# Kernel optimization log

Hardware: AMD Instinct MI355X
Metric: run time of the kernel (lower is better)

The kernel has to match this reference:

```python
import jax, jax.numpy as jnp
import numpy as np

N_NODES = 50000
DEG = 32
HEADS = 4
OUT_F = 16
IN_F = 64
NEG_SLOPE = 0.01  # jax.nn.leaky_relu default


def setup_inputs() -> dict:
    key = jax.random.key(0)
    k_adj, k_mask, k_q, k_qw, k_kw, k_aw = jax.random.split(key, 6)
    adj = jax.random.randint(k_adj, (N_NODES, DEG), 0, N_NODES)
    pad = jax.random.uniform(k_mask, (N_NODES, DEG)) < 0.1
    adj = jnp.where(pad, -1, adj)
    Q = jax.random.normal(k_q, (IN_F, N_NODES), dtype=jnp.float32)
    qw_scale = 2 * np.sqrt(6.0 / (IN_F + OUT_F * HEADS))
    kw_scale = qw_scale
    a_scale = 2 * np.sqrt(6.0 / (OUT_F + HEADS))
    query_weight = (jax.random.uniform(k_qw, (HEADS, OUT_F, IN_F)) - 0.5) * qw_scale
    key_weight = (jax.random.uniform(k_kw, (HEADS, OUT_F, IN_F)) - 0.5) * kw_scale
    attn_weight = (jax.random.uniform(k_aw, (HEADS, OUT_F)) - 0.5) * a_scale
    return {
        'adj': adj,
        'Q': Q,
        'query_weight': query_weight.astype(jnp.float32),
        'key_weight': key_weight.astype(jnp.float32),
        'attn_weight': attn_weight.astype(jnp.float32),
    }


def reference(adj, Q, query_weight, key_weight, attn_weight):
    # K defaults to Q (self-attention over graph)
    K = Q
    # project keys: [H, O, N], then gather neighbors -> [H, O, N, deg]
    Ko = jnp.einsum('hoi,in->hon', key_weight, K)[..., adj]
    # project queries: [H, O, N]
    Qo = jnp.einsum('hoi,in->hon', query_weight, Q)
    # per-edge pre-activation and attention logits
    X = jax.nn.leaky_relu(Qo[..., None] + Ko, negative_slope=NEG_SLOPE)
    X = jnp.einsum('honk,ho->hnk', X, attn_weight)  # [H, N, deg]
    X = jnp.where(adj == -1, -jnp.inf, X)
    # rows with zero valid neighbors -> zero logits (uniform softmax, masked later)
    X = jnp.where((adj != -1).sum(-1, keepdims=True) == 0, 0.0, X)
    attn = jax.nn.softmax(X, axis=-1)
    # weighted aggregate of gathered keys -> [H, O, N]
    return jnp.einsum('hnk,honk->hon', jnp.where(adj == -1, 0.0, attn), Ko)
```

## Files before the change

kernel.cpp:

```cpp
#include <hip/hip_runtime.h>
#include <math.h>

#define DEG 32
#define NHO 64
#define NPW 4
#define NPB 16

typedef short  frag8  __attribute__((ext_vector_type(8)));
typedef float  f32x4  __attribute__((ext_vector_type(4)));

template <int CTRL>
__device__ __forceinline__ float dpp_add(float v) {
    int t = __builtin_amdgcn_update_dpp(0, __float_as_int(v), CTRL, 0xF, 0xF, true);
    return v + __int_as_float(t);
}

__device__ __forceinline__ unsigned bf16_rne(float f) {
    unsigned u = __float_as_uint(f);
    return (u + 0x7fffu + ((u >> 16) & 1u)) >> 16;
}

__global__ __launch_bounds__(256) void proj_mfma_kernel(
    const float* __restrict__ Q,
    const float* __restrict__ Wq,
    const float* __restrict__ Wk,
    float* __restrict__ Pq,
    unsigned short* __restrict__ Pkb,
    int N)
{
    __shared__ unsigned qlds[64 * 33];
    __shared__ unsigned wlds[128 * 33];

    int t  = threadIdx.x;
    int n0 = blockIdx.x * 64;

    {
        int l    = t >> 1;
        int half = t & 1;
        const float* wr = (l < 64 ? Wq + (size_t)l * 64
                                  : Wk + (size_t)(l - 64) * 64) + half * 32;
#pragma unroll
        for (int r = 0; r < 16; r++) {
            float f0 = wr[2 * r], f1 = wr[2 * r + 1];
            wlds[l * 33 + half * 16 + r] = bf16_rne(f0) | (bf16_rne(f1) << 16);
        }
    }
    {
        int n  = t & 63;
        int gn = n0 + n;
        bool act = (gn < N);
#pragma unroll
        for (int r = 0; r < 8; r++) {
            int dp = (t >> 6) * 8 + r;
            int k  = dp * 2;
            float f0 = act ? Q[(size_t)k * N + gn] : 0.f;
            float f1 = act ? Q[(size_t)(k + 1) * N + gn] : 0.f;
            qlds[n * 33 + dp] = bf16_rne(f0) | (bf16_rne(f1) << 16);
        }
    }
    __syncthreads();

    int lane = t & 63;
    int w    = t >> 6;
    int li   = lane & 15;
    int quad = lane >> 4;

    f32x4 acc[8];
#pragma unroll
    for (int ot = 0; ot < 8; ot++) acc[ot] = (f32x4){0.f, 0.f, 0.f, 0.f};

#pragma unroll
    for (int ks = 0; ks < 2; ks++) {
        union { unsigned u[4]; frag8 f; } A;
        int abase = (w * 16 + li) * 33 + ks * 16 + quad * 4;
#pragma unroll
        for (int c = 0; c < 4; c++) A.u[c] = qlds[abase + c];
#pragma unroll
        for (int ot = 0; ot < 8; ot++) {
            union { unsigned u[4]; frag8 f; } B;
            int bbase = (ot * 16 + li) * 33 + ks * 16 + quad * 4;
#pragma unroll
            for (int c = 0; c < 4; c++) B.u[c] = wlds[bbase + c];
            acc[ot] = __builtin_amdgcn_mfma_f32_16x16x32_bf16(A.f, B.f, acc[ot],
                                                              0, 0, 0);
        }
    }

#pragma unroll
    for (int ot = 0; ot < 8; ot++) {
#pragma unroll
        for (int r = 0; r < 4; r++) {
            int node = n0 + w * 16 + quad * 4 + r;
            if (node < N) {
                float v = acc[ot][r];
                if (ot < 4) {
                    Pq[(size_t)node * NHO + ot * 16 + li] = v;
                } else {
                    Pkb[(size_t)node * NHO + (ot - 4) * 16 + li] =
                        (unsigned short)bf16_rne(v);
                }
            }
        }
    }
}

__global__ __launch_bounds__(256) void gat_kernel(
    const int*            __restrict__ adj,
    const float*          __restrict__ Pq,
    const unsigned short* __restrict__ Pkb,
    const float*          __restrict__ aw,
    float*                __restrict__ out,
    int N)
{
    __shared__ float tile[NHO][NPB + 1];

    int l    = threadIdx.x & 63;
    int wv   = threadIdx.x >> 6;
    int sl   = l & 31;
    int slot = l >> 5;

    const unsigned* Pk32 = (const unsigned*)Pkb;

    float2 awp = *(const float2*)(aw + 2 * sl);
    const float L2E = 1.44269504f;
    float c1_0 = 0.505f * L2E * awp.x, c2_0 = 0.495f * L2E * awp.x;
    float c1_1 = 0.505f * L2E * awp.y, c2_1 = 0.495f * L2E * awp.y;

    int bprm_it0 = slot * 64;
    int bprm_xor = (l ^ 32) * 4;

    int nbase = blockIdx.x * NPB + wv * NPW;

#pragma unroll 1
    for (int ni = 0; ni < NPW; ni++) {
        int n = nbase + ni;
        if (n < N) {
            float2 qp = *(const float2*)(Pq + (size_t)n * NHO + 2 * sl);
            int adjA  = adj[(size_t)n * DEG + sl];
            float c1q = fmaf(c1_1, qp.y, c1_0 * qp.x);

            int      jv[16];
            unsigned kvr[16];
#pragma unroll
            for (int t = 0; t < 16; t++) {
                int j = __builtin_amdgcn_ds_bpermute(bprm_it0 + t * 4, adjA);
                jv[t] = j;
                unsigned off = (((unsigned)(j < 0 ? 0 : j)) << 5) + sl;
                kvr[t] = Pk32[off];
            }

            float s = 0.f, a0 = 0.f, a1 = 0.f;
#pragma unroll
            for (int t = 0; t < 16; t++) {
                float kv0 = __uint_as_float(kvr[t] << 16);
                float kv1 = __uint_as_float(kvr[t] & 0xffff0000u);
                float x0  = qp.x + kv0;
                float x1  = qp.y + kv1;
                float c   = fmaf(c1_0, kv0, c1q);
                c = fmaf(c1_1, kv1, c);
                c = fmaf(c2_0, fabsf(x0), c);
                c = fmaf(c2_1, fabsf(x1), c);
                c = dpp_add<0xB1>(c);
                c = dpp_add<0x4E>(c);
                c = dpp_add<0x141>(c);
                float p = __builtin_amdgcn_exp2f(c);
                p = (jv[t] >= 0) ? p : 0.f;
                s += p;
                a0 = fmaf(p, kv0, a0);
                a1 = fmaf(p, kv1, a1);
            }

            s  += __int_as_float(__builtin_amdgcn_ds_bpermute(bprm_xor, __float_as_int(s)));
            a0 += __int_as_float(__builtin_amdgcn_ds_bpermute(bprm_xor, __float_as_int(a0)));
            a1 += __int_as_float(__builtin_amdgcn_ds_bpermute(bprm_xor, __float_as_int(a1)));

            float rs = (s > 0.f) ? __builtin_amdgcn_rcpf(s) : 0.f;
            if (slot == 0) {
                int col = wv * NPW + ni;
                tile[2 * sl + 0][col] = a0 * rs;
                tile[2 * sl + 1][col] = a1 * rs;
            }
        }
    }
    __syncthreads();

    int n0 = blockIdx.x * NPB;
    int lr = threadIdx.x >> 2;
    int c4 = threadIdx.x & 3;
    int nc = n0 + c4 * 4;
    float4 v = make_float4(tile[lr][c4 * 4 + 0], tile[lr][c4 * 4 + 1],
                           tile[lr][c4 * 4 + 2], tile[lr][c4 * 4 + 3]);
    if (nc + 3 < N) {
        *(float4*)(out + (size_t)lr * N + nc) = v;
    } else {
#pragma unroll
        for (int e = 0; e < 4; e++)
            if (nc + e < N) out[(size_t)lr * N + nc + e] = (&v.x)[e];
    }
}

extern "C" void kernel_launch(void* const* d_in, const int* in_sizes, int n_in,
                              void* d_out, int out_size, void* d_ws, size_t ws_size,
                              hipStream_t stream) {
    const int*   adj = (const int*)  d_in[0];
    const float* Q   = (const float*)d_in[1];
    const float* qw  = (const float*)d_in[2];
    const float* kw  = (const float*)d_in[3];
    const float* aw  = (const float*)d_in[4];
    float*       out = (float*)d_out;

    int N = in_sizes[0] / DEG;

    float*          Pq  = (float*)d_ws;
    unsigned short* Pkb = (unsigned short*)(Pq + (size_t)N * NHO);

    proj_mfma_kernel<<<(N + 63) / 64, 256, 0, stream>>>(Q, qw, kw, Pq, Pkb, N);

    gat_kernel<<<(N + NPB - 1) / NPB, 256, 0, stream>>>(adj, Pq, Pkb, aw, out, N);
}
```

Baseline: 111.6 us.

## Store query projection in bf16 and gather 4 features per lane

The query projection is now written in bf16 instead of fp32, which halves its workspace traffic. The GAT kernel remaps lanes so that each of 16 lanes handles 4 features (64-bit loads) and 4 lane groups each process 8 neighbors. This replaces 32 lanes of 2 features each with 2 groups of 16 neighbors. The per-edge reduction needs one fewer DPP step, while the cross-group reduction now takes two bpermute stages. Rounding the query projection to bf16 adds some precision loss.

```diff
diff --git a/kernel.cpp b/kernel.cpp
--- a/kernel.cpp
+++ b/kernel.cpp
@@ -24,7 +24,7 @@
     const float* __restrict__ Q,
     const float* __restrict__ Wq,
     const float* __restrict__ Wk,
-    float* __restrict__ Pq,
+    unsigned short* __restrict__ Pqb,
     unsigned short* __restrict__ Pkb,
     int N)
 {
@@ -92,13 +92,11 @@
         for (int r = 0; r < 4; r++) {
             int node = n0 + w * 16 + quad * 4 + r;
             if (node < N) {
-                float v = acc[ot][r];
-                if (ot < 4) {
-                    Pq[(size_t)node * NHO + ot * 16 + li] = v;
-                } else {
-                    Pkb[(size_t)node * NHO + (ot - 4) * 16 + li] =
-                        (unsigned short)bf16_rne(v);
-                }
+                unsigned short v = (unsigned short)bf16_rne(acc[ot][r]);
+                if (ot < 4)
+                    Pqb[(size_t)node * NHO + ot * 16 + li] = v;
+                else
+                    Pkb[(size_t)node * NHO + (ot - 4) * 16 + li] = v;
             }
         }
     }
@@ -106,7 +104,7 @@
 
 __global__ __launch_bounds__(256) void gat_kernel(
     const int*            __restrict__ adj,
-    const float*          __restrict__ Pq,
+    const unsigned short* __restrict__ Pqb,
     const unsigned short* __restrict__ Pkb,
     const float*          __restrict__ aw,
     float*                __restrict__ out,
@@ -116,18 +114,21 @@
 
     int l    = threadIdx.x & 63;
     int wv   = threadIdx.x >> 6;
-    int sl   = l & 31;
-    int slot = l >> 5;
-
-    const unsigned* Pk32 = (const unsigned*)Pkb;
-
-    float2 awp = *(const float2*)(aw + 2 * sl);
+    int sl   = l & 15;
+    int slot = l >> 4;
+
+    const uint2* Pk64 = (const uint2*)Pkb;
+    const uint2* Pq64 = (const uint2*)Pqb;
+
+    float4 awq = *(const float4*)(aw + 4 * sl);
     const float L2E = 1.44269504f;
-    float c1_0 = 0.505f * L2E * awp.x, c2_0 = 0.495f * L2E * awp.x;
-    float c1_1 = 0.505f * L2E * awp.y, c2_1 = 0.495f * L2E * awp.y;
-
-    int bprm_it0 = slot * 64;
-    int bprm_xor = (l ^ 32) * 4;
+    float c1_0 = 0.505f * L2E * awq.x, c2_0 = 0.495f * L2E * awq.x;
+    float c1_1 = 0.505f * L2E * awq.y, c2_1 = 0.495f * L2E * awq.y;
+    float c1_2 = 0.505f * L2E * awq.z, c2_2 = 0.495f * L2E * awq.z;
+    float c1_3 = 0.505f * L2E * awq.w, c2_3 = 0.495f * L2E * awq.w;
+
+    int bprm_x16 = (l ^ 16) * 4;
+    int bprm_x32 = (l ^ 32) * 4;
 
     int nbase = blockIdx.x * NPB + wv * NPW;
 
@@ -135,50 +136,73 @@
     for (int ni = 0; ni < NPW; ni++) {
         int n = nbase + ni;
         if (n < N) {
-            float2 qp = *(const float2*)(Pq + (size_t)n * NHO + 2 * sl);
-            int adjA  = adj[(size_t)n * DEG + sl];
-            float c1q = fmaf(c1_1, qp.y, c1_0 * qp.x);
-
-            int      jv[16];
-            unsigned kvr[16];
-#pragma unroll
-            for (int t = 0; t < 16; t++) {
-                int j = __builtin_amdgcn_ds_bpermute(bprm_it0 + t * 4, adjA);
+            uint2 qraw = Pq64[(size_t)n * 16 + sl];
+            float qp0 = __uint_as_float(qraw.x << 16);
+            float qp1 = __uint_as_float(qraw.x & 0xffff0000u);
+            float qp2 = __uint_as_float(qraw.y << 16);
+            float qp3 = __uint_as_float(qraw.y & 0xffff0000u);
+            int adjA  = adj[(size_t)n * DEG + (l & 31)];
+
+            float c1q = c1_0 * qp0;
+            c1q = fmaf(c1_1, qp1, c1q);
+            c1q = fmaf(c1_2, qp2, c1q);
+            c1q = fmaf(c1_3, qp3, c1q);
+
+            int   jv[8];
+            uint2 kvr[8];
+#pragma unroll
+            for (int t = 0; t < 8; t++) {
+                int j = __builtin_amdgcn_ds_bpermute((slot * 8 + t) * 4, adjA);
                 jv[t] = j;
-                unsigned off = (((unsigned)(j < 0 ? 0 : j)) << 5) + sl;
-                kvr[t] = Pk32[off];
-            }
-
-            float s = 0.f, a0 = 0.f, a1 = 0.f;
-#pragma unroll
-            for (int t = 0; t < 16; t++) {
-                float kv0 = __uint_as_float(kvr[t] << 16);
-                float kv1 = __uint_as_float(kvr[t] & 0xffff0000u);
-                float x0  = qp.x + kv0;
-                float x1  = qp.y + kv1;
-                float c   = fmaf(c1_0, kv0, c1q);
+                kvr[t] = Pk64[(size_t)(j < 0 ? 0 : j) * 16 + sl];
+            }
+
+            float s = 0.f, a0 = 0.f, a1 = 0.f, a2 = 0.f, a3 = 0.f;
+#pragma unroll
+            for (int t = 0; t < 8; t++) {
+                float kv0 = __uint_as_float(kvr[t].x << 16);
+                float kv1 = __uint_as_float(kvr[t].x & 0xffff0000u);
+                float kv2 = __uint_as_float(kvr[t].y << 16);
+                float kv3 = __uint_as_float(kvr[t].y & 0xffff0000u);
+                float x0 = qp0 + kv0, x1 = qp1 + kv1;
+                float x2 = qp2 + kv2, x3 = qp3 + kv3;
+                float c = fmaf(c1_0, kv0, c1q);
                 c = fmaf(c1_1, kv1, c);
+                c = fmaf(c1_2, kv2, c);
+                c = fmaf(c1_3, kv3, c);
                 c = fmaf(c2_0, fabsf(x0), c);
                 c = fmaf(c2_1, fabsf(x1), c);
+                c = fmaf(c2_2, fabsf(x2), c);
+                c = fmaf(c2_3, fabsf(x3), c);
                 c = dpp_add<0xB1>(c);
                 c = dpp_add<0x4E>(c);
-                c = dpp_add<0x141>(c);
                 float p = __builtin_amdgcn_exp2f(c);
                 p = (jv[t] >= 0) ? p : 0.f;
                 s += p;
                 a0 = fmaf(p, kv0, a0);
                 a1 = fmaf(p, kv1, a1);
-            }
-
-            s  += __int_as_float(__builtin_amdgcn_ds_bpermute(bprm_xor, __float_as_int(s)));
-            a0 += __int_as_float(__builtin_amdgcn_ds_bpermute(bprm_xor, __float_as_int(a0)));
-            a1 += __int_as_float(__builtin_amdgcn_ds_bpermute(bprm_xor, __float_as_int(a1)));
+                a2 = fmaf(p, kv2, a2);
+                a3 = fmaf(p, kv3, a3);
+            }
+
+            s  += __int_as_float(__builtin_amdgcn_ds_bpermute(bprm_x16, __float_as_int(s)));
+            a0 += __int_as_float(__builtin_amdgcn_ds_bpermute(bprm_x16, __float_as_int(a0)));
+            a1 += __int_as_float(__builtin_amdgcn_ds_bpermute(bprm_x16, __float_as_int(a1)));
+            a2 += __int_as_float(__builtin_amdgcn_ds_bpermute(bprm_x16, __float_as_int(a2)));
+            a3 += __int_as_float(__builtin_amdgcn_ds_bpermute(bprm_x16, __float_as_int(a3)));
+            s  += __int_as_float(__builtin_amdgcn_ds_bpermute(bprm_x32, __float_as_int(s)));
+            a0 += __int_as_float(__builtin_amdgcn_ds_bpermute(bprm_x32, __float_as_int(a0)));
+            a1 += __int_as_float(__builtin_amdgcn_ds_bpermute(bprm_x32, __float_as_int(a1)));
+            a2 += __int_as_float(__builtin_amdgcn_ds_bpermute(bprm_x32, __float_as_int(a2)));
+            a3 += __int_as_float(__builtin_amdgcn_ds_bpermute(bprm_x32, __float_as_int(a3)));
 
             float rs = (s > 0.f) ? __builtin_amdgcn_rcpf(s) : 0.f;
             if (slot == 0) {
                 int col = wv * NPW + ni;
-                tile[2 * sl + 0][col] = a0 * rs;
-                tile[2 * sl + 1][col] = a1 * rs;
+                tile[4 * sl + 0][col] = a0 * rs;
+                tile[4 * sl + 1][col] = a1 * rs;
+                tile[4 * sl + 2][col] = a2 * rs;
+                tile[4 * sl + 3][col] = a3 * rs;
             }
         }
     }
@@ -211,10 +235,10 @@
 
     int N = in_sizes[0] / DEG;
 
-    float*          Pq  = (float*)d_ws;
-    unsigned short* Pkb = (unsigned short*)(Pq + (size_t)N * NHO);
-
-    proj_mfma_kernel<<<(N + 63) / 64, 256, 0, stream>>>(Q, qw, kw, Pq, Pkb, N);
-
-    gat_kernel<<<(N + NPB - 1) / NPB, 256, 0, stream>>>(adj, Pq, Pkb, aw, out, N);
-}
+    unsigned short* Pqb = (unsigned short*)d_ws;
+    unsigned short* Pkb = Pqb + (size_t)N * NHO;
+
+    proj_mfma_kernel<<<(N + 63) / 64, 256, 0, stream>>>(Q, qw, kw, Pqb, Pkb, N);
+
+    gat_kernel<<<(N + NPB - 1) / NPB, 256, 0, stream>>>(adj, Pqb, Pkb, aw, out, N);
+}
```

New measurement: 107.6 us. 3.6% less time.

## Store projections in fp16 and compute edge logits with packed fdot2

Applied to the files above, without the earlier changes.

Q and K projections are now stored as fp16 instead of fp32 and bf16. The gather kernel is restructured so each wave handles four nodes at once, with 16 lanes per node and 4 features per lane, all 32 edges processed in chunks of 8. Logit pre-activations use packed half adds and fdot2 instructions, and the cross-lane reduction drops to two DPP steps. This halves Pq traffic, cuts per-edge ALU work and removes the serial per-node loop, at the cost of fp16 precision and range risk in the logits.

```diff
diff --git a/kernel.cpp b/kernel.cpp
--- a/kernel.cpp
+++ b/kernel.cpp
@@ -1,13 +1,22 @@
 #include <hip/hip_runtime.h>
+#include <hip/hip_fp16.h>
 #include <math.h>
 
 #define DEG 32
 #define NHO 64
-#define NPW 4
 #define NPB 16
 
-typedef short  frag8  __attribute__((ext_vector_type(8)));
-typedef float  f32x4  __attribute__((ext_vector_type(4)));
+typedef short    frag8 __attribute__((ext_vector_type(8)));
+typedef float    f32x4 __attribute__((ext_vector_type(4)));
+typedef _Float16 h2    __attribute__((ext_vector_type(2)));
+
+__device__ __forceinline__ h2 as_h2(unsigned u) {
+    union { unsigned u; h2 h; } x; x.u = u; return x.h;
+}
+__device__ __forceinline__ unsigned h2_add(unsigned a, unsigned b) {
+    h2 r = as_h2(a) + as_h2(b);
+    union { h2 h; unsigned u; } x; x.h = r; return x.u;
+}
 
 template <int CTRL>
 __device__ __forceinline__ float dpp_add(float v) {
@@ -24,8 +33,8 @@
     const float* __restrict__ Q,
     const float* __restrict__ Wq,
     const float* __restrict__ Wk,
-    float* __restrict__ Pq,
-    unsigned short* __restrict__ Pkb,
+    unsigned short* __restrict__ Pqh,
+    unsigned short* __restrict__ Pkh,
     int N)
 {
     __shared__ unsigned qlds[64 * 33];
@@ -92,13 +101,11 @@
         for (int r = 0; r < 4; r++) {
             int node = n0 + w * 16 + quad * 4 + r;
             if (node < N) {
-                float v = acc[ot][r];
-                if (ot < 4) {
-                    Pq[(size_t)node * NHO + ot * 16 + li] = v;
-                } else {
-                    Pkb[(size_t)node * NHO + (ot - 4) * 16 + li] =
-                        (unsigned short)bf16_rne(v);
-                }
+                unsigned short v = __half_as_ushort(__float2half(acc[ot][r]));
+                if (ot < 4)
+                    Pqh[(size_t)node * NHO + ot * 16 + li] = v;
+                else
+                    Pkh[(size_t)node * NHO + (ot - 4) * 16 + li] = v;
             }
         }
     }
@@ -106,8 +113,8 @@
 
 __global__ __launch_bounds__(256) void gat_kernel(
     const int*            __restrict__ adj,
-    const float*          __restrict__ Pq,
-    const unsigned short* __restrict__ Pkb,
+    const unsigned short* __restrict__ Pqh,
+    const unsigned short* __restrict__ Pkh,
     const float*          __restrict__ aw,
     float*                __restrict__ out,
     int N)
@@ -116,71 +123,77 @@
 
     int l    = threadIdx.x & 63;
     int wv   = threadIdx.x >> 6;
-    int sl   = l & 31;
-    int slot = l >> 5;
-
-    const unsigned* Pk32 = (const unsigned*)Pkb;
-
-    float2 awp = *(const float2*)(aw + 2 * sl);
+    int sl   = l & 15;
+    int slot = l >> 4;
+
+    const uint2* Pk64 = (const uint2*)Pkh;
+    const uint2* Pq64 = (const uint2*)Pqh;
+
+    float4 awq = *(const float4*)(aw + 4 * sl);
     const float L2E = 1.44269504f;
-    float c1_0 = 0.505f * L2E * awp.x, c2_0 = 0.495f * L2E * awp.x;
-    float c1_1 = 0.505f * L2E * awp.y, c2_1 = 0.495f * L2E * awp.y;
-
-    int bprm_it0 = slot * 64;
-    int bprm_xor = (l ^ 32) * 4;
-
-    int nbase = blockIdx.x * NPB + wv * NPW;
-
-#pragma unroll 1
-    for (int ni = 0; ni < NPW; ni++) {
-        int n = nbase + ni;
-        if (n < N) {
-            float2 qp = *(const float2*)(Pq + (size_t)n * NHO + 2 * sl);
-            int adjA  = adj[(size_t)n * DEG + sl];
-            float c1q = fmaf(c1_1, qp.y, c1_0 * qp.x);
-
-            int      jv[16];
-            unsigned kvr[16];
-#pragma unroll
-            for (int t = 0; t < 16; t++) {
-                int j = __builtin_amdgcn_ds_bpermute(bprm_it0 + t * 4, adjA);
-                jv[t] = j;
-                unsigned off = (((unsigned)(j < 0 ? 0 : j)) << 5) + sl;
-                kvr[t] = Pk32[off];
-            }
-
-            float s = 0.f, a0 = 0.f, a1 = 0.f;
-#pragma unroll
-            for (int t = 0; t < 16; t++) {
-                float kv0 = __uint_as_float(kvr[t] << 16);
-                float kv1 = __uint_as_float(kvr[t] & 0xffff0000u);
-                float x0  = qp.x + kv0;
-                float x1  = qp.y + kv1;
-                float c   = fmaf(c1_0, kv0, c1q);
-                c = fmaf(c1_1, kv1, c);
-                c = fmaf(c2_0, fabsf(x0), c);
-                c = fmaf(c2_1, fabsf(x1), c);
-                c = dpp_add<0xB1>(c);
-                c = dpp_add<0x4E>(c);
-                c = dpp_add<0x141>(c);
-                float p = __builtin_amdgcn_exp2f(c);
-                p = (jv[t] >= 0) ? p : 0.f;
-                s += p;
-                a0 = fmaf(p, kv0, a0);
-                a1 = fmaf(p, kv1, a1);
-            }
-
-            s  += __int_as_float(__builtin_amdgcn_ds_bpermute(bprm_xor, __float_as_int(s)));
-            a0 += __int_as_float(__builtin_amdgcn_ds_bpermute(bprm_xor, __float_as_int(a0)));
-            a1 += __int_as_float(__builtin_amdgcn_ds_bpermute(bprm_xor, __float_as_int(a1)));
-
-            float rs = (s > 0.f) ? __builtin_amdgcn_rcpf(s) : 0.f;
-            if (slot == 0) {
-                int col = wv * NPW + ni;
-                tile[2 * sl + 0][col] = a0 * rs;
-                tile[2 * sl + 1][col] = a1 * rs;
-            }
-        }
+    float c10 = 0.505f * L2E * awq.x, c20 = 0.495f * L2E * awq.x;
+    float c11 = 0.505f * L2E * awq.y, c21 = 0.495f * L2E * awq.y;
+    float c12 = 0.505f * L2E * awq.z, c22 = 0.495f * L2E * awq.z;
+    float c13 = 0.505f * L2E * awq.w, c23 = 0.495f * L2E * awq.w;
+    h2 c1a = {(_Float16)c10, (_Float16)c11};
+    h2 c1b = {(_Float16)c12, (_Float16)c13};
+    h2 c2a = {(_Float16)c20, (_Float16)c21};
+    h2 c2b = {(_Float16)c22, (_Float16)c23};
+
+    int n = blockIdx.x * NPB + wv * 4 + slot;
+    bool act = (n < N);
+    int nc_ = act ? n : 0;
+
+    uint2 qraw = Pq64[(size_t)nc_ * 16 + sl];
+    int2  av   = ((const int2*)adj)[(size_t)nc_ * 16 + sl];
+
+    float c1q = __builtin_amdgcn_fdot2(c1a, as_h2(qraw.x),
+                 __builtin_amdgcn_fdot2(c1b, as_h2(qraw.y), 0.f, false), false);
+
+    float s = 0.f, a0 = 0.f, a1 = 0.f, a2 = 0.f, a3 = 0.f;
+
+#pragma unroll
+    for (int ch = 0; ch < 4; ch++) {
+        int   jv[8];
+        uint2 kvr[8];
+#pragma unroll
+        for (int t8 = 0; t8 < 8; t8++) {
+            int t = ch * 8 + t8;
+            int addr = (slot * 16 + (t >> 1)) * 4;
+            int j = __builtin_amdgcn_ds_bpermute(addr, (t & 1) ? av.y : av.x);
+            jv[t8] = j;
+            kvr[t8] = Pk64[(size_t)(j < 0 ? 0 : j) * 16 + sl];
+        }
+#pragma unroll
+        for (int t8 = 0; t8 < 8; t8++) {
+            unsigned k01 = kvr[t8].x, k23 = kvr[t8].y;
+            unsigned x01 = h2_add(k01, qraw.x) & 0x7fff7fffu;
+            unsigned x23 = h2_add(k23, qraw.y) & 0x7fff7fffu;
+            float c = c1q;
+            c = __builtin_amdgcn_fdot2(c1a, as_h2(k01), c, false);
+            c = __builtin_amdgcn_fdot2(c1b, as_h2(k23), c, false);
+            c = __builtin_amdgcn_fdot2(c2a, as_h2(x01), c, false);
+            c = __builtin_amdgcn_fdot2(c2b, as_h2(x23), c, false);
+            c = dpp_add<0xB1>(c);
+            c = dpp_add<0x4E>(c);
+            float p = __builtin_amdgcn_exp2f(c);
+            p = (jv[t8] >= 0) ? p : 0.f;
+            s += p;
+            h2 kva = as_h2(k01), kvb = as_h2(k23);
+            a0 = fmaf(p, (float)kva[0], a0);
+            a1 = fmaf(p, (float)kva[1], a1);
+            a2 = fmaf(p, (float)kvb[0], a2);
+            a3 = fmaf(p, (float)kvb[1], a3);
+        }
+    }
+
+    if (act) {
+        float rs = (s > 0.f) ? __builtin_amdgcn_rcpf(s) : 0.f;
+        int col = wv * 4 + slot;
+        tile[4 * sl + 0][col] = a0 * rs;
+        tile[4 * sl + 1][col] = a1 * rs;
+        tile[4 * sl + 2][col] = a2 * rs;
+        tile[4 * sl + 3][col] = a3 * rs;
     }
     __syncthreads();
 
@@ -211,10 +224,10 @@
 
     int N = in_sizes[0] / DEG;
 
-    float*          Pq  = (float*)d_ws;
-    unsigned short* Pkb = (unsigned short*)(Pq + (size_t)N * NHO);
-
-    proj_mfma_kernel<<<(N + 63) / 64, 256, 0, stream>>>(Q, qw, kw, Pq, Pkb, N);
-
-    gat_kernel<<<(N + NPB - 1) / NPB, 256, 0, stream>>>(adj, Pq, Pkb, aw, out, N);
-}
+    unsigned short* Pqh = (unsigned short*)d_ws;
+    unsigned short* Pkh = Pqh + (size_t)N * NHO;
+
+    proj_mfma_kernel<<<(N + 63) / 64, 256, 0, stream>>>(Q, qw, kw, Pqh, Pkh, N);
+
+    gat_kernel<<<(N + NPB - 1) / NPB, 256, 0, stream>>>(adj, Pqh, Pkh, aw, out, N);
+}
```

After: 107.9 us. 1.03x faster.
